# Performance work log

Hardware: AMD Instinct MI355X
Metric: run time of the kernel (lower is better)

Reference implementation:

```python
import jax, jax.numpy as jnp
import numpy as np

NINP, NHID, NOUT = 400, 600, 400
HS = NHID + NOUT          # h_size = nhid + nout
NLEVELS, K, AUX_FREQ = 40, 2, 20
DILATION = [1]


def setup_inputs() -> dict:
    key = jax.random.key(0)
    ks = jax.random.split(key, 6)
    B, T = 8, 256
    bound = 0.01  # matches init_weights normal_(0, 0.01)
    return {
        "X": jax.random.normal(ks[0], (B, NINP, T), jnp.float32),
        "hid": jax.random.normal(ks[1], (B, HS, 1), jnp.float32),
        "cell": jax.random.normal(ks[2], (B, HS, 1), jnp.float32),
        "w1": jax.random.normal(ks[3], (4 * HS, NINP, K), jnp.float32) * bound,
        "w2": jax.random.normal(ks[4], (4 * HS, HS, K), jnp.float32) * bound,
        "b2": jax.random.normal(ks[5], (4 * HS,), jnp.float32) * bound,
    }


def _conv1d(x, w, d):
    # x: [B, Cin, T_padded], w: [Cout, Cin, K] -> [B, Cout, T]
    return jax.lax.conv_general_dilated(
        x, w, window_strides=(1,), padding='VALID', rhs_dilation=(d,),
        dimension_numbers=('NCH', 'OIH', 'NCH'))


def _forward(X, hid, cell, w1, w2, b2):
    B, _, T = X.shape
    ht = jnp.zeros((B, HS, T), X.dtype)
    ct = jnp.zeros((B, HS, T), X.dtype)

    # Input-side convolution is weight-tied and X never changes across levels,
    # so (like the torch dict cache) compute it once per distinct dilation.
    conv1 = {}
    for d in set(DILATION):
        pad = (K - 1) * d
        xp = jnp.pad(X, ((0, 0), (0, 0), (pad, 0)))
        conv1[d] = _conv1d(xp, w1, d)

    aux = []
    for i in range(NLEVELS):
        d = DILATION[i % len(DILATION)]
        pad = (K - 1) * d
        # causal left-pad of the hidden stream, filled with the initial hid
        z1 = jnp.concatenate([jnp.broadcast_to(hid, (B, HS, pad)), ht], axis=2)
        out = conv1[d] + _conv1d(z1, w2, d) + b2[None, :, None]  # [B, 4*HS, T]
        # shifted cell state, first d steps filled with the initial cell
        ct_1 = jnp.concatenate(
            [jnp.broadcast_to(cell, (B, HS, d)), ct[:, :, :-d]], axis=2)
        it = jax.nn.sigmoid(out[:, :HS])
        ot = jax.nn.sigmoid(out[:, HS:2 * HS])
        gt = jnp.tanh(out[:, 2 * HS:3 * HS])
        ft = jax.nn.sigmoid(out[:, 3 * HS:])
        ct = ft * ct_1 + it * gt
        ht = ot * jnp.tanh(ct)
        if i % AUX_FREQ == AUX_FREQ - 1:
            aux.append(ht[:, -NOUT:])  # [B, nout, T]

    out_main = jnp.transpose(ht[:, -NOUT:], (0, 2, 1))            # [B, T, nout]
    hc = (ht[:, :, -1:], ct[:, :, -1:])                            # ([B,HS,1], [B,HS,1])
    aux_outs = jnp.transpose(jnp.stack(aux, axis=0), (1, 0, 3, 2))  # [B, n_aux, T, nout]
    return out_main, hc, aux_outs


def reference(X, hid, cell, w1, w2, b2):
    return _forward(X, hid, cell, w1, w2, b2)
```

## Files before the change

### kernel.cpp

```cpp
#include <hip/hip_runtime.h>
#include <hip/hip_bf16.h>
#include <math.h>

typedef __bf16 bf16;
typedef __bf16 bf16x8 __attribute__((ext_vector_type(8)));
typedef __bf16 bf16x4 __attribute__((ext_vector_type(4)));
typedef float f32x4 __attribute__((ext_vector_type(4)));
typedef unsigned int u32;
typedef u32 u32x4 __attribute__((ext_vector_type(4)));

#define NINP 400
#define HS   1000
#define HP   1024
#define B_   8
#define T_   256
#define NT   2048
#define M_   4096

#define HT_OFF   819200
#define CT_OFF   827200
#define AUX_OFF  835200

#define ALO  0
#define AHI  4096
#define HSB  8192
#define BUFE 12352

typedef __attribute__((address_space(1))) const void gvoid;
typedef __attribute__((address_space(3))) void lvoid;

__device__ __forceinline__ void async_copy16(void* lds, const void* g) {
  __builtin_amdgcn_global_load_lds((gvoid*)g, (lvoid*)lds, 16, 0, 0);
}

__device__ __forceinline__ float sigm(float x) { return 1.0f / (1.0f + expf(-x)); }


__global__ void repack_w1(const float* __restrict__ w1, bf16* __restrict__ W1q) {
  int idx = blockIdx.x * 256 + threadIdx.x;
  if (idx >= M_ * 1024) return;
  int pm = idx >> 10, k = idx & 1023;
  int g = (pm >> 4) & 3;
  int h = (pm >> 7) * 32 + ((pm >> 6) & 1) * 16 + (pm & 15);
  float v = 0.0f;
  if (h < HS) {
    int c = g * HS + h;
    if (k < 512) { if (k < NINP) v = w1[(size_t)c * (NINP * 2) + k * 2 + 0]; }
    else { int j = k - 512; if (j < NINP) v = w1[(size_t)c * (NINP * 2) + j * 2 + 1]; }
  }
  W1q[idx] = (bf16)v;
}

__global__ void repack_w2(const float* __restrict__ w2, bf16* __restrict__ W2q) {
  int idx = blockIdx.x * 256 + threadIdx.x;
  if (idx >= M_ * 2048) return;
  int pm = idx >> 11, k = idx & 2047;
  int g = (pm >> 4) & 3;
  int h = (pm >> 7) * 32 + ((pm >> 6) & 1) * 16 + (pm & 15);
  float v = 0.0f;
  if (h < HS) {
    int c = g * HS + h;
    if (k < HP) { if (k < HS) v = w2[(size_t)c * (HS * 2) + k * 2 + 0]; }
    else { int j = k - HP; if (j < HS) v = w2[(size_t)c * (HS * 2) + j * 2 + 1]; }
  }
  W2q[idx] = (bf16)v;
}

__global__ void build_xs(const float* __restrict__ X, bf16* __restrict__ XSg) {
  int idx = blockIdx.x * 256 + threadIdx.x;
  if (idx >= (NT + 1) * 512) return;
  int row = idx >> 9, k = idx & 511;
  float v = 0.0f;
  if (row > 0 && k < NINP) {
    int n = row - 1;
    int b = n >> 8, t = n & (T_ - 1);
    v = X[((size_t)b * NINP + k) * T_ + t];
  }
  XSg[idx] = (bf16)v;
}

__global__ void build_hc(const float* __restrict__ hid, const float* __restrict__ cell,
                         bf16* __restrict__ hidp, float* __restrict__ cellp) {
  int idx = blockIdx.x * 256 + threadIdx.x;
  if (idx >= B_ * HP) return;
  int b = idx >> 10, k = idx & (HP - 1);
  hidp[idx]  = (k < HS) ? (bf16)hid[b * HS + k] : (bf16)0.0f;
  cellp[idx] = (k < HS) ? cell[b * HS + k] : 0.0f;
}


template <bool GATED>
__global__ __launch_bounds__(256, 2) void gemm_step(
    const bf16* __restrict__ A,
    const bf16* __restrict__ Bsrc,
    const bf16* __restrict__ hidp,
    const bf16* __restrict__ CbIn,
    bf16* __restrict__ CbOut,
    const float* __restrict__ b2,
    const bf16* __restrict__ ctprev,
    const float* __restrict__ cellp,
    bf16* __restrict__ ctnew,
    bf16* __restrict__ Hnew,
    int KH, int BS) {
  __shared__ bf16 SMF[2 * BUFE];

  const int tid = threadIdx.x;
  const int lane = tid & 63;
  const int w = tid >> 6;
  const int mh = w >> 1, nh = w & 1;
  const int quad = lane >> 4, col = lane & 15;
  const int K = KH * 2;

  const int L = blockIdx.y * gridDim.x + blockIdx.x;
  const int bm = (L & 7) * 4 + (L >> 7);
  const int n0 = ((L >> 3) & 15) * 128;

  bf16x4 cb0[4], cb1[4], cb2[4], cb3[4];
  if (GATED) {
#pragma unroll
    for (int nt = 0; nt < 4; ++nt) {
      const int n = n0 + nh * 64 + nt * 16 + col;
      const size_t cb = (size_t)n * 4096 + (size_t)(bm * 128 + mh * 64) + quad * 4;
      cb0[nt] = *(const bf16x4*)&CbIn[cb + 0];
      cb1[nt] = *(const bf16x4*)&CbIn[cb + 16];
      cb2[nt] = *(const bf16x4*)&CbIn[cb + 32];
      cb3[nt] = *(const bf16x4*)&CbIn[cb + 48];
    }
  }

  const int colh = col >> 1;
  const int slotA = ((quad + 4 * (col & 1) + (colh & 7)) & 7) * 8;
  const int baseA   = (mh * 32 + colh) * 64 + slotA;
  const int baseBhi = HSB + 64 + (nh * 32 + colh) * 64 + slotA;
  int baseLo[4];
#pragma unroll
  for (int nt = 0; nt < 4; ++nt) {
    const int r = nh * 64 + nt * 16 + col - 1;
    const int pr = r >> 1;
    baseLo[nt] = HSB + (pr + 1) * 64 + (((quad + 4 * (r & 1) + (pr & 7)) & 7) * 8);
  }

  const bf16* paLo[2];
  const bf16* pbs[2];
#pragma unroll
  for (int l = 0; l < 2; ++l) {
    const int f = l * 256 + tid;
    const int pr = f >> 3, sl = f & 7;
    const int u = (sl - (pr & 7)) & 7;
    const int r = 2 * pr + (u >> 2), k8 = u & 3;
    paLo[l] = A + (size_t)(bm * 128 + r) * K + k8 * 8;
    pbs[l]  = Bsrc + (size_t)(n0 + r) * BS + k8 * 8;
  }
  const bf16* zsrc = GATED ? (hidp + (size_t)(n0 >> 8) * HP) : (Bsrc - BS);
  const bf16* pbm1 = ((n0 & 255) == 0) ? zsrc : (Bsrc + (size_t)(n0 - 1) * BS);
  const bf16* pbm1l = pbm1 + (((lane + 1) & 7) & 3) * 8;

  f32x4 acc[4][4];
#pragma unroll
  for (int i = 0; i < 4; ++i)
#pragma unroll
    for (int j = 0; j < 4; ++j) acc[i][j] = (f32x4){0.f, 0.f, 0.f, 0.f};

  auto stage = [&](int buf, int p2) {
    const int bufo = buf * BUFE;
#pragma unroll
    for (int l = 0; l < 2; ++l) {
      const int d = (l * 256 + w * 64) * 8;
      async_copy16(&SMF[bufo + ALO + d],      paLo[l] + p2 * 32);
      async_copy16(&SMF[bufo + AHI + d],      paLo[l] + KH + p2 * 32);
      async_copy16(&SMF[bufo + HSB + 64 + d], pbs[l] + p2 * 32);
    }
    if (lane < 8) async_copy16(&SMF[bufo + HSB], pbm1l + p2 * 32);
  };

  const int NP = KH >> 5;

  auto kpair = [&](int p2, int buf) {
    const int bufo = buf * BUFE;
    {
      bf16x8 av[4], bv[4];
#pragma unroll
      for (int mt = 0; mt < 4; ++mt)
        av[mt] = *(const bf16x8*)&SMF[bufo + ALO + baseA + mt * 512];
#pragma unroll
      for (int nt = 0; nt < 4; ++nt)
        bv[nt] = *(const bf16x8*)&SMF[bufo + baseLo[nt]];
      __builtin_amdgcn_s_barrier();
      asm volatile("s_waitcnt lgkmcnt(0)" ::: "memory");
      __builtin_amdgcn_sched_barrier(0);
      __builtin_amdgcn_s_setprio(1);
#pragma unroll
      for (int mt = 0; mt < 4; ++mt)
#pragma unroll
        for (int nt = 0; nt < 4; ++nt)
          acc[mt][nt] = __builtin_amdgcn_mfma_f32_16x16x32_bf16(av[mt], bv[nt], acc[mt][nt], 0, 0, 0);
      __builtin_amdgcn_s_setprio(0);
      __builtin_amdgcn_s_barrier();
    }
    {
      bf16x8 av[4], bv[4];
#pragma unroll
      for (int mt = 0; mt < 4; ++mt)
        av[mt] = *(const bf16x8*)&SMF[bufo + AHI + baseA + mt * 512];
#pragma unroll
      for (int nt = 0; nt < 4; ++nt)
        bv[nt] = *(const bf16x8*)&SMF[bufo + baseBhi + nt * 512];
      asm volatile("s_waitcnt lgkmcnt(0)" ::: "memory");
      __builtin_amdgcn_sched_barrier(0);
      __builtin_amdgcn_s_barrier();
      if (p2 + 2 < NP) {
        stage(buf, p2 + 2);
        asm volatile("s_waitcnt vmcnt(7)" ::: "memory");
      } else {
        asm volatile("s_waitcnt vmcnt(0)" ::: "memory");
      }
      __builtin_amdgcn_sched_barrier(0);
      __builtin_amdgcn_s_setprio(1);
#pragma unroll
      for (int mt = 0; mt < 4; ++mt)
#pragma unroll
        for (int nt = 0; nt < 4; ++nt)
          acc[mt][nt] = __builtin_amdgcn_mfma_f32_16x16x32_bf16(av[mt], bv[nt], acc[mt][nt], 0, 0, 0);
      __builtin_amdgcn_s_setprio(0);
      __builtin_amdgcn_s_barrier();
    }
  };

  stage(0, 0);
  stage(1, 1);
  __syncthreads();

  for (int p = 0; p < NP; p += 2) {
    kpair(p, 0);
    kpair(p + 1, 1);
  }
  __syncthreads();

  if (!GATED) {
    bf16 (*Csh)[128] = (bf16(*)[128])&SMF[0];
#pragma unroll
    for (int mt = 0; mt < 4; ++mt) {
#pragma unroll
      for (int nt = 0; nt < 4; ++nt) {
        const int nloc = nh * 64 + nt * 16 + col;
        bf16x4 v;
#pragma unroll
        for (int j = 0; j < 4; ++j) {
          const int h = bm * 32 + mh * 16 + quad * 4 + j;
          const float bias = (h < HS) ? b2[mt * HS + h] : 0.0f;
          v[j] = (bf16)(acc[mt][nt][j] + bias);
        }
        *(bf16x4*)&Csh[nloc][mh * 64 + mt * 16 + quad * 4] = v;
      }
    }
    __syncthreads();
#pragma unroll
    for (int i2 = 0; i2 < 8; ++i2) {
      const int idx = i2 * 256 + tid;
      const int rrow = idx >> 4, off = idx & 15;
      *(u32x4*)&CbOut[(size_t)(n0 + rrow) * 4096 + bm * 128 + off * 8] =
          *(const u32x4*)&Csh[rrow][off * 8];
    }
  } else {
    bf16 (*Hsh)[32] = (bf16(*)[32])&SMF[0];
#pragma unroll
    for (int nt = 0; nt < 4; ++nt) {
      const int nloc = nh * 64 + nt * 16 + col;
      const int n = n0 + nloc;
      const int b = n >> 8;
      const int t = n & (T_ - 1);
      bf16x4 hv;
#pragma unroll
      for (int j = 0; j < 4; ++j) {
        const int h = bm * 32 + mh * 16 + quad * 4 + j;
        const float ci = acc[0][nt][j] + (float)cb0[nt][j];
        const float co = acc[1][nt][j] + (float)cb1[nt][j];
        const float cg = acc[2][nt][j] + (float)cb2[nt][j];
        const float cf = acc[3][nt][j] + (float)cb3[nt][j];
        const float ctold = (t == 0) ? cellp[b * HP + h]
                                     : (float)ctprev[(size_t)h * NT + (n - 1)];
        const float cn = sigm(cf) * ctold + sigm(ci) * tanhf(cg);
        ctnew[(size_t)h * NT + n] = (bf16)cn;
        hv[j] = (bf16)(sigm(co) * tanhf(cn));
      }
      *(bf16x4*)&Hsh[nloc][mh * 16 + quad * 4] = hv;
    }
    __syncthreads();
#pragma unroll
    for (int i2 = 0; i2 < 2; ++i2) {
      const int idx = i2 * 256 + tid;
      const int rrow = idx >> 2, off = idx & 3;
      *(u32x4*)&Hnew[(size_t)(n0 + rrow) * HP + bm * 32 + off * 8] =
          *(const u32x4*)&Hsh[rrow][off * 8];
    }
  }
}


__global__ void aux_kernel(const bf16* __restrict__ H, float* __restrict__ out, int s) {
  int idx = blockIdx.x * 256 + threadIdx.x;
  if (idx >= NT * 100) return;
  int n = idx / 100;
  int o = (idx % 100) * 4;
  int b = n >> 8, t = n & (T_ - 1);
  bf16x4 v = *(const bf16x4*)&H[(size_t)n * HP + 600 + o];
  f32x4 f = {(float)v[0], (float)v[1], (float)v[2], (float)v[3]};
  *(f32x4*)&out[AUX_OFF + ((size_t)((b * 2 + s) * T_ + t)) * 400 + o] = f;
}

__global__ void final_kernel(const bf16* __restrict__ H, const bf16* __restrict__ ct,
                             float* __restrict__ out) {
  int idx = blockIdx.x * 256 + threadIdx.x;
  if (idx < NT * 100) {
    int n = idx / 100;
    int o = (idx % 100) * 4;
    int b = n >> 8, t = n & (T_ - 1);
    bf16x4 v = *(const bf16x4*)&H[(size_t)n * HP + 600 + o];
    f32x4 f = {(float)v[0], (float)v[1], (float)v[2], (float)v[3]};
    *(f32x4*)&out[(size_t)n * 400 + o] = f;
    *(f32x4*)&out[AUX_OFF + ((size_t)((b * 2 + 1) * T_ + t)) * 400 + o] = f;
  } else {
    int j = idx - NT * 100;
    if (j < 8000) {
      int b = j / 1000, h = j % 1000;
      out[HT_OFF + j] = (float)H[(size_t)(b * T_ + 255) * HP + h];
    } else if (j < 16000) {
      int jj = j - 8000;
      int b = jj / 1000, h = jj % 1000;
      out[CT_OFF + jj] = (float)ct[(size_t)h * NT + b * T_ + 255];
    }
  }
}


extern "C" void kernel_launch(void* const* d_in, const int* in_sizes, int n_in,
                              void* d_out, int out_size, void* d_ws, size_t ws_size,
                              hipStream_t stream) {
  const float* X    = (const float*)d_in[0];
  const float* hid  = (const float*)d_in[1];
  const float* cell = (const float*)d_in[2];
  const float* w1   = (const float*)d_in[3];
  const float* w2   = (const float*)d_in[4];
  const float* b2   = (const float*)d_in[5];
  float* out = (float*)d_out;

  char* ws = (char*)d_ws;
  size_t off = 0;
  auto alloc = [&](size_t bytes) {
    void* p = ws + off;
    off += (bytes + 255) & ~(size_t)255;
    return p;
  };
  bf16* W2q    = (bf16*)alloc((size_t)M_ * 2048 * 2);
  bf16* CbP    = (bf16*)alloc((size_t)NT * M_ * 2);
  bf16* Hb0    = (bf16*)alloc((size_t)NT * HP * 2);
  bf16* ctb0   = (bf16*)alloc((size_t)HP * NT * 2);
  bf16* hidp   = (bf16*)alloc((size_t)B_ * HP * 2);
  float* cellp = (float*)alloc((size_t)B_ * HP * 4);
  char* R = (char*)alloc((size_t)12 * 1024 * 1024);
  bf16* W1q  = (bf16*)R;
  bf16* XSg  = (bf16*)(R + (size_t)8 * 1024 * 1024);
  bf16* ctb1 = (bf16*)R;
  bf16* Hb1  = (bf16*)(R + (size_t)4 * 1024 * 1024);

  bf16* Hb[2]  = {Hb0, Hb1};
  bf16* ctb[2] = {ctb0, ctb1};

  hipMemsetAsync(Hb[0], 0, (size_t)NT * HP * 2, stream);
  hipMemsetAsync(ctb[0], 0, (size_t)HP * NT * 2, stream);

  repack_w1<<<(M_ * 1024) / 256, 256, 0, stream>>>(w1, W1q);
  repack_w2<<<(M_ * 2048) / 256, 256, 0, stream>>>(w2, W2q);
  build_xs<<<((NT + 1) * 512) / 256, 256, 0, stream>>>(X, XSg);
  build_hc<<<(B_ * HP) / 256, 256, 0, stream>>>(hid, cell, hidp, cellp);

  dim3 grid(NT / 128, M_ / 128);
  gemm_step<false><<<grid, 256, 0, stream>>>(W1q, XSg + 512, nullptr, nullptr, CbP, b2,
                                             nullptr, nullptr, nullptr, nullptr,
                                             512, 512);
  for (int i = 0; i < 40; ++i) {
    int p = i & 1;
    gemm_step<true><<<grid, 256, 0, stream>>>(W2q, Hb[p], hidp, CbP, nullptr, nullptr,
                                              ctb[p], cellp, ctb[p ^ 1], Hb[p ^ 1],
                                              1024, 1024);
    if (i == 19) aux_kernel<<<800, 256, 0, stream>>>(Hb[p ^ 1], out, 0);
  }
  final_kernel<<<(NT * 100 + 16000 + 255) / 256, 256, 0, stream>>>(Hb[0], ctb[0], out);
}
```

Measured before the change: 2.011 ms.

## Load B operand directly from global into registers, stage only A in LDS

Reworks the GEMM main loop so only the weight tile A is staged through LDS via async copies, while the activation operand B is read straight from global memory into registers, including the causal shifted tap. The loop becomes a double-buffered 64-wide K iteration with compile-time K, and the explicit shifted-row staging and many barriers go away. This cuts LDS footprint and synchronisation but relies on the cache for B reuse across waves and uses full vmcnt(0) waits, which may expose global latency. The non-gated call now passes XSg without the offset, so the shifted-tap indexing is handled differently.

```diff
diff --git a/kernel.cpp b/kernel.cpp
--- a/kernel.cpp
+++ b/kernel.cpp
@@ -20,11 +20,6 @@
 #define HT_OFF   819200
 #define CT_OFF   827200
 #define AUX_OFF  835200
-
-#define ALO  0
-#define AHI  4096
-#define HSB  8192
-#define BUFE 12352
 
 typedef __attribute__((address_space(1))) const void gvoid;
 typedef __attribute__((address_space(3))) void lvoid;
@@ -89,7 +84,7 @@
 }
 
 
-template <bool GATED>
+template <bool GATED, int K>
 __global__ __launch_bounds__(256, 2) void gemm_step(
     const bf16* __restrict__ A,
     const bf16* __restrict__ Bsrc,
@@ -100,16 +95,19 @@
     const bf16* __restrict__ ctprev,
     const float* __restrict__ cellp,
     bf16* __restrict__ ctnew,
-    bf16* __restrict__ Hnew,
-    int KH, int BS) {
-  __shared__ bf16 SMF[2 * BUFE];
+    bf16* __restrict__ Hnew) {
+  constexpr int KH = K / 2;
+  constexpr int BS = KH;
+  constexpr int NIT = K / 64;
+  __shared__ bf16 As[2][128][64];
 
   const int tid = threadIdx.x;
   const int lane = tid & 63;
   const int w = tid >> 6;
   const int mh = w >> 1, nh = w & 1;
+  const int dr = lane >> 3, c8 = lane & 7;
+  const int swo = ((c8 - dr) & 7) * 8;
   const int quad = lane >> 4, col = lane & 15;
-  const int K = KH * 2;
 
   const int L = blockIdx.y * gridDim.x + blockIdx.x;
   const int bm = (L & 7) * 4 + (L >> 7);
@@ -128,32 +126,26 @@
     }
   }
 
-  const int colh = col >> 1;
-  const int slotA = ((quad + 4 * (col & 1) + (colh & 7)) & 7) * 8;
-  const int baseA   = (mh * 32 + colh) * 64 + slotA;
-  const int baseBhi = HSB + 64 + (nh * 32 + colh) * 64 + slotA;
-  int baseLo[4];
+  const bf16* pa[4];
+#pragma unroll
+  for (int j = 0; j < 4; ++j)
+    pa[j] = A + (size_t)(bm * 128 + j * 32 + w * 8 + dr) * K + swo;
+
+  const bf16* bvbase[2][4];
 #pragma unroll
   for (int nt = 0; nt < 4; ++nt) {
-    const int r = nh * 64 + nt * 16 + col - 1;
-    const int pr = r >> 1;
-    baseLo[nt] = HSB + (pr + 1) * 64 + (((quad + 4 * (r & 1) + (pr & 7)) & 7) * 8);
-  }
-
-  const bf16* paLo[2];
-  const bf16* pbs[2];
-#pragma unroll
-  for (int l = 0; l < 2; ++l) {
-    const int f = l * 256 + tid;
-    const int pr = f >> 3, sl = f & 7;
-    const int u = (sl - (pr & 7)) & 7;
-    const int r = 2 * pr + (u >> 2), k8 = u & 3;
-    paLo[l] = A + (size_t)(bm * 128 + r) * K + k8 * 8;
-    pbs[l]  = Bsrc + (size_t)(n0 + r) * BS + k8 * 8;
-  }
-  const bf16* zsrc = GATED ? (hidp + (size_t)(n0 >> 8) * HP) : (Bsrc - BS);
-  const bf16* pbm1 = ((n0 & 255) == 0) ? zsrc : (Bsrc + (size_t)(n0 - 1) * BS);
-  const bf16* pbm1l = pbm1 + (((lane + 1) & 7) & 3) * 8;
+    const int n = n0 + nh * 64 + nt * 16 + col;
+    const int t = n & (T_ - 1);
+    if (GATED) {
+      bvbase[1][nt] = Bsrc + (size_t)n * BS + quad * 8;
+      bvbase[0][nt] = (t == 0) ? (hidp + (size_t)(n >> 8) * HP + quad * 8)
+                               : (Bsrc + (size_t)(n - 1) * BS + quad * 8);
+    } else {
+      bvbase[0][nt] = (t == 0) ? (Bsrc + quad * 8)
+                               : (Bsrc + (size_t)n * BS + quad * 8);
+      bvbase[1][nt] = Bsrc + (size_t)(n + 1) * BS + quad * 8;
+    }
+  }
 
   f32x4 acc[4][4];
 #pragma unroll
@@ -161,31 +153,31 @@
 #pragma unroll
     for (int j = 0; j < 4; ++j) acc[i][j] = (f32x4){0.f, 0.f, 0.f, 0.f};
 
-  auto stage = [&](int buf, int p2) {
-    const int bufo = buf * BUFE;
-#pragma unroll
-    for (int l = 0; l < 2; ++l) {
-      const int d = (l * 256 + w * 64) * 8;
-      async_copy16(&SMF[bufo + ALO + d],      paLo[l] + p2 * 32);
-      async_copy16(&SMF[bufo + AHI + d],      paLo[l] + KH + p2 * 32);
-      async_copy16(&SMF[bufo + HSB + 64 + d], pbs[l] + p2 * 32);
-    }
-    if (lane < 8) async_copy16(&SMF[bufo + HSB], pbm1l + p2 * 32);
+  auto stage = [&](int buf, int it) {
+#pragma unroll
+    for (int j = 0; j < 4; ++j)
+      async_copy16(&As[buf][j * 32 + w * 8][0], pa[j] + it * 64);
   };
 
-  const int NP = KH >> 5;
-
-  auto kpair = [&](int p2, int buf) {
-    const int bufo = buf * BUFE;
-    {
-      bf16x8 av[4], bv[4];
-#pragma unroll
-      for (int mt = 0; mt < 4; ++mt)
-        av[mt] = *(const bf16x8*)&SMF[bufo + ALO + baseA + mt * 512];
+  auto loadB = [&](bf16x8 (&dst)[2][4], int it) {
+    const int tap = (it * 64 >= KH) ? 1 : 0;
+    const int koff = it * 64 - tap * KH;
+#pragma unroll
+    for (int h = 0; h < 2; ++h)
 #pragma unroll
       for (int nt = 0; nt < 4; ++nt)
-        bv[nt] = *(const bf16x8*)&SMF[bufo + baseLo[nt]];
-      __builtin_amdgcn_s_barrier();
+        dst[h][nt] = *(const bf16x8*)(bvbase[tap][nt] + koff + h * 32);
+  };
+
+  auto phases = [&](int buf, bf16x8 (&bvv)[2][4]) {
+#pragma unroll
+    for (int h = 0; h < 2; ++h) {
+      bf16x8 av[4];
+#pragma unroll
+      for (int mt = 0; mt < 4; ++mt) {
+        const int rA = mh * 64 + mt * 16 + col;
+        av[mt] = *(const bf16x8*)&As[buf][rA][((h * 4 + quad + rA) & 7) * 8];
+      }
       asm volatile("s_waitcnt lgkmcnt(0)" ::: "memory");
       __builtin_amdgcn_sched_barrier(0);
       __builtin_amdgcn_s_setprio(1);
@@ -193,51 +185,29 @@
       for (int mt = 0; mt < 4; ++mt)
 #pragma unroll
         for (int nt = 0; nt < 4; ++nt)
-          acc[mt][nt] = __builtin_amdgcn_mfma_f32_16x16x32_bf16(av[mt], bv[nt], acc[mt][nt], 0, 0, 0);
+          acc[mt][nt] = __builtin_amdgcn_mfma_f32_16x16x32_bf16(av[mt], bvv[h][nt], acc[mt][nt], 0, 0, 0);
       __builtin_amdgcn_s_setprio(0);
-      __builtin_amdgcn_s_barrier();
-    }
-    {
-      bf16x8 av[4], bv[4];
-#pragma unroll
-      for (int mt = 0; mt < 4; ++mt)
-        av[mt] = *(const bf16x8*)&SMF[bufo + AHI + baseA + mt * 512];
-#pragma unroll
-      for (int nt = 0; nt < 4; ++nt)
-        bv[nt] = *(const bf16x8*)&SMF[bufo + baseBhi + nt * 512];
-      asm volatile("s_waitcnt lgkmcnt(0)" ::: "memory");
-      __builtin_amdgcn_sched_barrier(0);
-      __builtin_amdgcn_s_barrier();
-      if (p2 + 2 < NP) {
-        stage(buf, p2 + 2);
-        asm volatile("s_waitcnt vmcnt(7)" ::: "memory");
-      } else {
-        asm volatile("s_waitcnt vmcnt(0)" ::: "memory");
-      }
-      __builtin_amdgcn_sched_barrier(0);
-      __builtin_amdgcn_s_setprio(1);
-#pragma unroll
-      for (int mt = 0; mt < 4; ++mt)
-#pragma unroll
-        for (int nt = 0; nt < 4; ++nt)
-          acc[mt][nt] = __builtin_amdgcn_mfma_f32_16x16x32_bf16(av[mt], bv[nt], acc[mt][nt], 0, 0, 0);
-      __builtin_amdgcn_s_setprio(0);
-      __builtin_amdgcn_s_barrier();
     }
   };
 
+  bf16x8 bv0[2][4], bv1[2][4];
   stage(0, 0);
-  stage(1, 1);
+  loadB(bv0, 0);
+#pragma unroll
+  for (int it = 0; it < NIT; it += 2) {
+    asm volatile("s_waitcnt vmcnt(0)" ::: "memory");
+    __builtin_amdgcn_s_barrier();
+    if (it + 1 < NIT) { stage(1, it + 1); loadB(bv1, it + 1); }
+    phases(0, bv0);
+    asm volatile("s_waitcnt vmcnt(0)" ::: "memory");
+    __builtin_amdgcn_s_barrier();
+    if (it + 2 < NIT) { stage(0, it + 2); loadB(bv0, it + 2); }
+    phases(1, bv1);
+  }
   __syncthreads();
 
-  for (int p = 0; p < NP; p += 2) {
-    kpair(p, 0);
-    kpair(p + 1, 1);
-  }
-  __syncthreads();
-
   if (!GATED) {
-    bf16 (*Csh)[128] = (bf16(*)[128])&SMF[0];
+    bf16 (*Csh)[128] = (bf16(*)[128])&As[0][0][0];
 #pragma unroll
     for (int mt = 0; mt < 4; ++mt) {
 #pragma unroll
@@ -262,7 +232,7 @@
           *(const u32x4*)&Csh[rrow][off * 8];
     }
   } else {
-    bf16 (*Hsh)[32] = (bf16(*)[32])&SMF[0];
+    bf16 (*Hsh)[32] = (bf16(*)[32])&As[0][0][0];
 #pragma unroll
     for (int nt = 0; nt < 4; ++nt) {
       const int nloc = nh * 64 + nt * 16 + col;
@@ -375,14 +345,12 @@
   build_hc<<<(B_ * HP) / 256, 256, 0, stream>>>(hid, cell, hidp, cellp);
 
   dim3 grid(NT / 128, M_ / 128);
-  gemm_step<false><<<grid, 256, 0, stream>>>(W1q, XSg + 512, nullptr, nullptr, CbP, b2,
-                                             nullptr, nullptr, nullptr, nullptr,
-                                             512, 512);
+  gemm_step<false, 1024><<<grid, 256, 0, stream>>>(W1q, XSg, nullptr, nullptr, CbP, b2,
+                                                   nullptr, nullptr, nullptr, nullptr);
   for (int i = 0; i < 40; ++i) {
     int p = i & 1;
-    gemm_step<true><<<grid, 256, 0, stream>>>(W2q, Hb[p], hidp, CbP, nullptr, nullptr,
-                                              ctb[p], cellp, ctb[p ^ 1], Hb[p ^ 1],
-                                              1024, 1024);
+    gemm_step<true, 2048><<<grid, 256, 0, stream>>>(W2q, Hb[p], hidp, CbP, nullptr, nullptr,
+                                                    ctb[p], cellp, ctb[p ^ 1], Hb[p ^ 1]);
     if (i == 19) aux_kernel<<<800, 256, 0, stream>>>(Hb[p ^ 1], out, 0);
   }
   final_kernel<<<(NT * 100 + 16000 + 255) / 256, 256, 0, stream>>>(Hb[0], ctb[0], out);
```

Result: slower. 3.363 ms (+67.2%).
